# Optimization experiments

Measured on AMD Instinct MI355X. Metric: run time of the kernel, lower is better.

The kernel has to match this reference:

```python
import jax, jax.numpy as jnp
import numpy as np

B, S, D, H = 2, 2048, 1024, 16
DK = D // H
SCALE = 1.0 / np.sqrt(DK).astype(np.float32)


def setup_inputs() -> dict:
    key = jax.random.key(0)
    ks = jax.random.split(key, 7)
    std = 1.0 / np.sqrt(D).astype(np.float32)
    return {
        "query": jax.random.normal(ks[0], (B, S, D), jnp.float32),
        "key": jax.random.normal(ks[1], (B, S, D), jnp.float32),
        "value": jax.random.normal(ks[2], (B, S, D), jnp.float32),
        "Wq": jax.random.normal(ks[3], (D, D), jnp.float32) * std,
        "Wk": jax.random.normal(ks[4], (D, D), jnp.float32) * std,
        "Wv": jax.random.normal(ks[5], (D, D), jnp.float32) * std,
        "Wo": jax.random.normal(ks[6], (D, D), jnp.float32) * std,
    }


def _split_heads(x):
    # [B, S, D] -> [B, H, S, DK]
    return x.reshape(B, S, H, DK).transpose(0, 2, 1, 3)


def reference(query, key, value, Wq, Wk, Wv, Wo):
    Q = _split_heads(query @ Wq)
    K = _split_heads(key @ Wk)
    V = _split_heads(value @ Wv)
    # explicit full-score attention, as in the original (mask=None, dropout off)
    scores = jnp.einsum("bhqd,bhkd->bhqk", Q, K) * SCALE
    attn = jax.nn.softmax(scores, axis=-1)
    out = jnp.einsum("bhqk,bhkd->bhqd", attn, V)
    out = out.transpose(0, 2, 1, 3).reshape(B, S, D)  # merge heads
    return out @ Wo
```

## Files before the change

### kernel.cpp

```cpp
#include <hip/hip_runtime.h>

#define B_ 2
#define S_ 2048
#define D_ 1024
#define H_ 16

typedef unsigned short u16;
typedef unsigned long long u64;
typedef __bf16 bf16x8 __attribute__((ext_vector_type(8)));
typedef float f32x4 __attribute__((ext_vector_type(4)));
typedef unsigned short u16x8 __attribute__((ext_vector_type(8)));
typedef unsigned short u16x4 __attribute__((ext_vector_type(4)));
typedef unsigned uint4v __attribute__((ext_vector_type(4)));

__device__ __forceinline__ unsigned swz128(unsigned o) {
  return o ^ (((o >> 7) & 7) << 4);
}
__device__ __forceinline__ unsigned swz256(unsigned o) {
  return o ^ (((o >> 8) & 7) << 4);
}

__device__ __forceinline__ unsigned xcd_swz(unsigned id, unsigned cpx) {
  return (id & 7) * cpx + (id >> 3);
}

__device__ __forceinline__ void gload_lds16(const void* g, void* l) {
  __builtin_amdgcn_global_load_lds(
      (const __attribute__((address_space(1))) unsigned*)g,
      (__attribute__((address_space(3))) unsigned*)l, 16, 0, 0);
}

__device__ __forceinline__ u16 f2bf(float f) {
  union { float f; unsigned u; } v;
  v.f = f;
  unsigned u = v.u;
  return (u16)((u + 0x7fffu + ((u >> 16) & 1u)) >> 16);
}

__device__ __forceinline__ unsigned cvtpk(float lo, float hi) {
  unsigned d;
  asm("v_cvt_pk_bf16_f32 %0, %1, %2" : "=v"(d) : "v"(lo), "v"(hi));
  return d;
}

__device__ __forceinline__ float max3f(float a, float b, float c) {
  float d;
  asm("v_max3_f32 %0, %1, %2, %3" : "=v"(d) : "v"(a), "v"(b), "v"(c));
  return d;
}

struct T4 { const float* in[4]; u16* out[4]; };
__global__ __launch_bounds__(256) void transpose_w4(T4 p) {
  __shared__ u16 t[64][65];
  const float* in = p.in[blockIdx.z];
  u16* out = p.out[blockIdx.z];
  int r0 = blockIdx.y * 64, c0 = blockIdx.x * 64;
  for (int i = threadIdx.x; i < 4096; i += 256) {
    int r = i >> 6, c = i & 63;
    t[r][c] = f2bf(in[(size_t)(r0 + r) * 1024 + c0 + c]);
  }
  __syncthreads();
  for (int i = threadIdx.x; i < 4096; i += 256) {
    int r = i >> 6, c = i & 63;
    out[(size_t)(c0 + r) * 1024 + r0 + c] = t[c][r];
  }
}

struct QKV { const float* A[3]; const u16* BT[3]; u16* C[2]; u16* VT; };
__global__ __launch_bounds__(256) void gemm_qkv(QKV p) {
  constexpr int K = 1024, N = 1024;
  __shared__ __align__(16) u16 lbuf[2][128 * 64];
  const int tid = threadIdx.x, lane = tid & 63, w = tid >> 6;
  const int wr = w >> 1, wc = w & 1;
  const int z = blockIdx.z;
  const int m0 = blockIdx.x * 128, n0 = blockIdx.y * 128;
  const int g = lane >> 4, c16 = lane & 15;
  f32x4 acc[4][4] = {};
  const float* Af = p.A[z] + (size_t)m0 * K;
  const char* Bb = (const char*)(p.BT[z] + (size_t)n0 * K);
  char* lAb = (char*)lbuf[0];
  char* lBb = (char*)lbuf[1];
  for (int kt = 0; kt < K; kt += 64) {
    for (int c = 0; c < 4; ++c) {
      unsigned o = c * 4096 + tid * 16;
      unsigned u = swz128(o);
      gload_lds16(Bb + (size_t)(u >> 7) * (K * 2) + kt * 2 + (u & 127), lBb + o);
    }
    for (int c = 0; c < 4; ++c) {
      unsigned o = c * 4096 + tid * 16;
      unsigned row = o >> 7, kc = (o & 127) >> 1;
      const float* s = Af + (size_t)row * K + kt + kc;
      float4 f0 = *(const float4*)s;
      float4 f1 = *(const float4*)(s + 4);
      uint4v d;
      d[0] = cvtpk(f0.x, f0.y);
      d[1] = cvtpk(f0.z, f0.w);
      d[2] = cvtpk(f1.x, f1.y);
      d[3] = cvtpk(f1.z, f1.w);
      *(uint4v*)(lAb + swz128(o)) = d;
    }
    asm volatile("s_waitcnt vmcnt(0)" ::: "memory");
    __syncthreads();
    for (int ks = 0; ks < 2; ++ks) {
      bf16x8 af[4], bf[4];
      for (int i = 0; i < 4; ++i) {
        unsigned row = wr * 64 + i * 16 + c16;
        unsigned o = row * 128 + ks * 64 + g * 16;
        af[i] = *(const bf16x8*)(lAb + (o ^ ((row & 7) << 4)));
      }
      for (int j = 0; j < 4; ++j) {
        unsigned row = wc * 64 + j * 16 + c16;
        unsigned o = row * 128 + ks * 64 + g * 16;
        bf[j] = *(const bf16x8*)(lBb + (o ^ ((row & 7) << 4)));
      }
      for (int i = 0; i < 4; ++i)
        for (int j = 0; j < 4; ++j)
          acc[i][j] = __builtin_amdgcn_mfma_f32_16x16x32_bf16(af[i], bf[j],
                                                              acc[i][j], 0, 0, 0);
    }
    __syncthreads();
  }
  if (z < 2) {
    u16* C = p.C[z];
    for (int i = 0; i < 4; ++i)
      for (int j = 0; j < 4; ++j) {
        int row = m0 + wr * 64 + i * 16 + g * 4;
        int col = n0 + wc * 64 + j * 16 + c16;
        for (int r = 0; r < 4; ++r)
          C[(size_t)(row + r) * N + col] = f2bf(acc[i][j][r]);
      }
  } else {
    char* Tb = (char*)lbuf;
    for (int i = 0; i < 4; ++i)
      for (int j = 0; j < 4; ++j) {
        unsigned s_local = wr * 64 + i * 16 + g * 4;
        unsigned dk_col = wc * 64 + j * 16 + c16;
        unsigned o = dk_col * 256 + s_local * 2;
        u16x4 ov;
        ov[0] = f2bf(acc[i][j][0]);
        ov[1] = f2bf(acc[i][j][1]);
        ov[2] = f2bf(acc[i][j][2]);
        ov[3] = f2bf(acc[i][j][3]);
        *(u16x4*)(Tb + swz256(o)) = ov;
      }
    __syncthreads();
    const int b = m0 >> 11, s0blk = m0 & 2047;
    for (int c = 0; c < 8; ++c) {
      unsigned idx = c * 4096 + tid * 16;
      unsigned row = idx >> 8, off = idx & 255;
      int h = (n0 + (int)row) >> 6, dk = (n0 + (int)row) & 63;
      int bh = b * 16 + h;
      char* dst = (char*)p.VT + (((size_t)bh * 64 + dk) * S_ + s0blk) * 2 + off;
      *(u16x8*)dst = *(const u16x8*)(Tb + swz256(idx));
    }
  }
}

__global__ __launch_bounds__(256) void gemm_bt_f32(const u16* __restrict__ A,
                                                   const u16* __restrict__ BT,
                                                   float* __restrict__ C) {
  constexpr int K = 1024, N = 1024;
  __shared__ __align__(16) u16 lA[128 * 64];
  __shared__ __align__(16) u16 lB[64 * 64];
  const int tid = threadIdx.x, lane = tid & 63, w = tid >> 6;
  const int wr = w >> 1, wc = w & 1;
  const int m0 = blockIdx.x * 128, n0 = blockIdx.y * 64;
  const int g = lane >> 4, c16 = lane & 15;
  f32x4 acc[4][2] = {};
  const char* Ab = (const char*)(A + (size_t)m0 * K);
  const char* Bb = (const char*)(BT + (size_t)n0 * K);
  char* lAb = (char*)lA;
  char* lBb = (char*)lB;
  for (int kt = 0; kt < K; kt += 64) {
    for (int c = 0; c < 4; ++c) {
      unsigned o = w * 4096 + c * 1024 + lane * 16;
      unsigned u = swz128(o);
      gload_lds16(Ab + (size_t)(u >> 7) * (K * 2) + kt * 2 + (u & 127),
                  lAb + w * 4096 + c * 1024);
    }
    for (int c = 0; c < 2; ++c) {
      unsigned o = w * 2048 + c * 1024 + lane * 16;
      unsigned u = swz128(o);
      gload_lds16(Bb + (size_t)(u >> 7) * (K * 2) + kt * 2 + (u & 127),
                  lBb + w * 2048 + c * 1024);
    }
    asm volatile("s_waitcnt vmcnt(0)" ::: "memory");
    __syncthreads();
    for (int ks = 0; ks < 2; ++ks) {
      bf16x8 af[4], bf[2];
      for (int i = 0; i < 4; ++i) {
        unsigned row = wr * 64 + i * 16 + c16;
        unsigned o = row * 128 + ks * 64 + g * 16;
        af[i] = *(const bf16x8*)(lAb + (o ^ ((row & 7) << 4)));
      }
      for (int j = 0; j < 2; ++j) {
        unsigned row = wc * 32 + j * 16 + c16;
        unsigned o = row * 128 + ks * 64 + g * 16;
        bf[j] = *(const bf16x8*)(lBb + (o ^ ((row & 7) << 4)));
      }
      for (int i = 0; i < 4; ++i)
        for (int j = 0; j < 2; ++j)
          acc[i][j] = __builtin_amdgcn_mfma_f32_16x16x32_bf16(af[i], bf[j],
                                                              acc[i][j], 0, 0, 0);
    }
    __syncthreads();
  }
  for (int i = 0; i < 4; ++i)
    for (int j = 0; j < 2; ++j) {
      int row = m0 + wr * 64 + i * 16 + g * 4;
      int col = n0 + wc * 32 + j * 16 + c16;
      for (int r = 0; r < 4; ++r)
        C[(size_t)(row + r) * N + col] = acc[i][j][r];
    }
}

__global__ __launch_bounds__(256) void flash_attn(const u16* __restrict__ Q,
                                                  const u16* __restrict__ K,
                                                  const u16* __restrict__ VT,
                                                  u16* __restrict__ O) {
  __shared__ __align__(16) u16 lP[64 * 64];
  __shared__ __align__(16) u16 lK[2][64 * 64];
  __shared__ __align__(16) u16 lV[2][64 * 64];
  const int tid = threadIdx.x, lane = tid & 63, w = tid >> 6;
  const int g = lane >> 4, c16 = lane & 15;
  unsigned id = blockIdx.x + blockIdx.y * gridDim.x;
  unsigned sw = xcd_swz(id, 128);
  const int q0 = (sw & 31) * 64;
  const int bh = sw >> 5, b = bh >> 4, h = bh & 15;
  const char* Qb = (const char*)(Q + (size_t)(b * S_ + q0) * D_ + h * 64);
  const char* Kb = (const char*)(K + (size_t)b * S_ * D_ + h * 64);
  const char* Vb = (const char*)(VT + (size_t)bh * 64 * S_);
  char* lPb = (char*)lP;
  char* lKb = (char*)lK;
  char* lVb = (char*)lV;

  const unsigned mask = (c16 & 7) << 4;
  const unsigned fb0 = c16 * 128 + ((g * 16) ^ mask);
  const unsigned fb1 = c16 * 128 + ((64 + g * 16) ^ mask);
  unsigned uo[2];
  for (int c = 0; c < 2; ++c) uo[c] = swz128(w * 2048 + c * 1024 + lane * 16);

  for (int c = 0; c < 2; ++c) {
    unsigned u = uo[c];
    unsigned dst = w * 2048 + c * 1024;
    gload_lds16(Qb + (size_t)(u >> 7) * (D_ * 2) + (u & 127), lPb + dst);
    gload_lds16(Kb + (size_t)(u >> 7) * (D_ * 2) + (u & 127), lKb + dst);
    gload_lds16(Vb + (size_t)(u >> 7) * (S_ * 2) + (u & 127), lVb + dst);
  }
  float m_run = -INFINITY, l_run = 0.f;
  f32x4 oacc[4] = {};
  asm volatile("s_waitcnt vmcnt(0)" ::: "memory");
  __syncthreads();
  bf16x8 qf[2];
  qf[0] = *(const bf16x8*)(lPb + w * 2048 + fb0);
  qf[1] = *(const bf16x8*)(lPb + w * 2048 + fb1);
  const float SC2 = 0.125f * 1.44269504088896340736f;
  const unsigned qrow = w * 16 + c16;
  const unsigned pw = qrow * 128 + ((g * 8) ^ (mask & 16));
  const unsigned mh = mask & 96;
  int cur = 0;
  for (int kv0 = 0; kv0 < S_; kv0 += 64, cur ^= 1) {
    const char* curK = lKb + cur * 8192;
    const char* curV = lVb + cur * 8192;
    if (kv0 + 64 < S_) {
      char* nK = lKb + (cur ^ 1) * 8192;
      char* nV = lVb + (cur ^ 1) * 8192;
      for (int c = 0; c < 2; ++c) {
        unsigned u = uo[c];
        unsigned dst = w * 2048 + c * 1024;
        gload_lds16(Kb + (size_t)(kv0 + 64 + (u >> 7)) * (D_ * 2) + (u & 127),
                    nK + dst);
        gload_lds16(Vb + (size_t)(u >> 7) * (S_ * 2) + (size_t)(kv0 + 64) * 2 + (u & 127),
                    nV + dst);
      }
    }
    f32x4 s[4] = {};
    __builtin_amdgcn_s_setprio(1);
    for (int j = 0; j < 4; ++j) {
      bf16x8 kf = *(const bf16x8*)(curK + fb0 + j * 2048);
      s[j] = __builtin_amdgcn_mfma_f32_16x16x32_bf16(kf, qf[0], s[j], 0, 0, 0);
    }
    for (int j = 0; j < 4; ++j) {
      bf16x8 kf = *(const bf16x8*)(curK + fb1 + j * 2048);
      s[j] = __builtin_amdgcn_mfma_f32_16x16x32_bf16(kf, qf[1], s[j], 0, 0, 0);
    }
    __builtin_amdgcn_s_setprio(0);
    float t0 = max3f(s[0][0], s[0][1], s[0][2]);
    float t1 = max3f(s[0][3], s[1][0], s[1][1]);
    float t2 = max3f(s[1][2], s[1][3], s[2][0]);
    float t3 = max3f(s[2][1], s[2][2], s[2][3]);
    float t4 = max3f(s[3][0], s[3][1], s[3][2]);
    float rm = fmaxf(max3f(t0, t1, t2), max3f(t3, t4, s[3][3]));
    rm = fmaxf(rm, __shfl_xor(rm, 16));
    rm = fmaxf(rm, __shfl_xor(rm, 32));
    if (!__all((rm - m_run) * SC2 <= 8.0f)) {
      float mn = fmaxf(m_run, rm);
      float sc = exp2f((m_run - mn) * SC2);
      l_run *= sc;
      for (int i = 0; i < 4; ++i) oacc[i] *= sc;
      m_run = mn;
    }
    float rsj[4];
    for (int j = 0; j < 4; ++j) {
      float p0 = exp2f((s[j][0] - m_run) * SC2);
      float p1 = exp2f((s[j][1] - m_run) * SC2);
      float p2 = exp2f((s[j][2] - m_run) * SC2);
      float p3 = exp2f((s[j][3] - m_run) * SC2);
      rsj[j] = (p0 + p1) + (p2 + p3);
      unsigned w0 = cvtpk(p0, p1);
      unsigned w1 = cvtpk(p2, p3);
      *(u64*)(lPb + pw + ((unsigned)(j * 32) ^ mh)) = (u64)w0 | ((u64)w1 << 32);
    }
    l_run += (rsj[0] + rsj[1]) + (rsj[2] + rsj[3]);
    __builtin_amdgcn_s_setprio(1);
    {
      bf16x8 pf0 = *(const bf16x8*)(lPb + w * 2048 + fb0);
      for (int i = 0; i < 4; ++i) {
        bf16x8 vf = *(const bf16x8*)(curV + fb0 + i * 2048);
        oacc[i] = __builtin_amdgcn_mfma_f32_16x16x32_bf16(vf, pf0, oacc[i], 0, 0, 0);
      }
      bf16x8 pf1 = *(const bf16x8*)(lPb + w * 2048 + fb1);
      for (int i = 0; i < 4; ++i) {
        bf16x8 vf = *(const bf16x8*)(curV + fb1 + i * 2048);
        oacc[i] = __builtin_amdgcn_mfma_f32_16x16x32_bf16(vf, pf1, oacc[i], 0, 0, 0);
      }
    }
    __builtin_amdgcn_s_setprio(0);
    asm volatile("s_waitcnt vmcnt(0)" ::: "memory");
    __syncthreads();
  }
  l_run += __shfl_xor(l_run, 16);
  l_run += __shfl_xor(l_run, 32);
  float inv = 1.f / l_run;
  int q = q0 + w * 16 + c16;
  u16* orow = O + (size_t)(b * S_ + q) * D_ + h * 64;
  for (int i = 0; i < 4; ++i) {
    unsigned e0 = cvtpk(oacc[i][0] * inv, oacc[i][1] * inv);
    unsigned e1 = cvtpk(oacc[i][2] * inv, oacc[i][3] * inv);
    *(u64*)(orow + i * 16 + g * 4) = (u64)e0 | ((u64)e1 << 32);
  }
}

extern "C" void kernel_launch(void* const* d_in, const int* in_sizes, int n_in,
                              void* d_out, int out_size, void* d_ws, size_t ws_size,
                              hipStream_t stream) {
  const float* q_in = (const float*)d_in[0];
  const float* k_in = (const float*)d_in[1];
  const float* v_in = (const float*)d_in[2];
  const float* Wq = (const float*)d_in[3];
  const float* Wk = (const float*)d_in[4];
  const float* Wv = (const float*)d_in[5];
  const float* Wo = (const float*)d_in[6];
  u16* ws = (u16*)d_ws;
  const size_t WSZ = (size_t)1024 * 1024;
  const size_t TSZ = (size_t)B_ * S_ * D_;
  u16* WqT = ws;
  u16* WkT = ws + WSZ;
  u16* WvT = ws + 2 * WSZ;
  u16* WoT = ws + 3 * WSZ;
  u16* Qb = ws + 4 * WSZ;
  u16* Kb = Qb + TSZ;
  u16* VTb = Kb + TSZ;
  u16* Ob = VTb + TSZ;
  dim3 tb(256);
  T4 tw = {{Wq, Wk, Wv, Wo}, {WqT, WkT, WvT, WoT}};
  transpose_w4<<<dim3(16, 16, 4), tb, 0, stream>>>(tw);
  QKV gq = {{q_in, k_in, v_in}, {WqT, WkT, WvT}, {Qb, Kb}, VTb};
  gemm_qkv<<<dim3(32, 8, 3), tb, 0, stream>>>(gq);
  flash_attn<<<dim3(32, 32), tb, 0, stream>>>(Qb, Kb, VTb, Ob);
  gemm_bt_f32<<<dim3(32, 16), tb, 0, stream>>>(Ob, WoT, (float*)d_out);
}
```

Baseline: 153.7 us.

## Split attention KV range in two with a merge kernel, single-buffer LDS

Flash attention now splits each query tile's KV sequence into two halves processed by separate blocks, doubling the grid to 2048 blocks. Each block writes unnormalized partial outputs (bf16) and its running max and sum, and a new merge_o kernel combines the two halves and normalizes. K/V LDS staging drops from double-buffered prefetch to a single buffer loaded after compute with a full wait, which shrinks LDS per block. It targets better occupancy and CU fill, but adds a kernel launch, extra partial-output traffic, bf16 rounding of the unnormalized partials, and loses the load/compute overlap.

```diff
diff --git a/kernel.cpp b/kernel.cpp
--- a/kernel.cpp
+++ b/kernel.cpp
@@ -35,6 +35,12 @@
   v.f = f;
   unsigned u = v.u;
   return (u16)((u + 0x7fffu + ((u >> 16) & 1u)) >> 16);
+}
+
+__device__ __forceinline__ float bf2f(u16 x) {
+  union { unsigned u; float f; } v;
+  v.u = ((unsigned)x) << 16;
+  return v.f;
 }
 
 __device__ __forceinline__ unsigned cvtpk(float lo, float hi) {
@@ -217,16 +223,18 @@
 __global__ __launch_bounds__(256) void flash_attn(const u16* __restrict__ Q,
                                                   const u16* __restrict__ K,
                                                   const u16* __restrict__ VT,
-                                                  u16* __restrict__ O) {
+                                                  u16* __restrict__ pO,
+                                                  float2* __restrict__ pML) {
   __shared__ __align__(16) u16 lP[64 * 64];
-  __shared__ __align__(16) u16 lK[2][64 * 64];
-  __shared__ __align__(16) u16 lV[2][64 * 64];
+  __shared__ __align__(16) u16 lK[64 * 64];
+  __shared__ __align__(16) u16 lV[64 * 64];
   const int tid = threadIdx.x, lane = tid & 63, w = tid >> 6;
   const int g = lane >> 4, c16 = lane & 15;
-  unsigned id = blockIdx.x + blockIdx.y * gridDim.x;
-  unsigned sw = xcd_swz(id, 128);
+  unsigned sw = xcd_swz(blockIdx.x, 256);
   const int q0 = (sw & 31) * 64;
-  const int bh = sw >> 5, b = bh >> 4, h = bh & 15;
+  const int half = (sw >> 5) & 1;
+  const int bh = sw >> 6, b = bh >> 4, h = bh & 15;
+  const int kv_base = half * (S_ / 2);
   const char* Qb = (const char*)(Q + (size_t)(b * S_ + q0) * D_ + h * 64);
   const char* Kb = (const char*)(K + (size_t)b * S_ * D_ + h * 64);
   const char* Vb = (const char*)(VT + (size_t)bh * 64 * S_);
@@ -244,8 +252,8 @@
     unsigned u = uo[c];
     unsigned dst = w * 2048 + c * 1024;
     gload_lds16(Qb + (size_t)(u >> 7) * (D_ * 2) + (u & 127), lPb + dst);
-    gload_lds16(Kb + (size_t)(u >> 7) * (D_ * 2) + (u & 127), lKb + dst);
-    gload_lds16(Vb + (size_t)(u >> 7) * (S_ * 2) + (u & 127), lVb + dst);
+    gload_lds16(Kb + (size_t)(kv_base + (u >> 7)) * (D_ * 2) + (u & 127), lKb + dst);
+    gload_lds16(Vb + (size_t)(u >> 7) * (S_ * 2) + (size_t)kv_base * 2 + (u & 127), lVb + dst);
   }
   float m_run = -INFINITY, l_run = 0.f;
   f32x4 oacc[4] = {};
@@ -258,30 +266,15 @@
   const unsigned qrow = w * 16 + c16;
   const unsigned pw = qrow * 128 + ((g * 8) ^ (mask & 16));
   const unsigned mh = mask & 96;
-  int cur = 0;
-  for (int kv0 = 0; kv0 < S_; kv0 += 64, cur ^= 1) {
-    const char* curK = lKb + cur * 8192;
-    const char* curV = lVb + cur * 8192;
-    if (kv0 + 64 < S_) {
-      char* nK = lKb + (cur ^ 1) * 8192;
-      char* nV = lVb + (cur ^ 1) * 8192;
-      for (int c = 0; c < 2; ++c) {
-        unsigned u = uo[c];
-        unsigned dst = w * 2048 + c * 1024;
-        gload_lds16(Kb + (size_t)(kv0 + 64 + (u >> 7)) * (D_ * 2) + (u & 127),
-                    nK + dst);
-        gload_lds16(Vb + (size_t)(u >> 7) * (S_ * 2) + (size_t)(kv0 + 64) * 2 + (u & 127),
-                    nV + dst);
-      }
-    }
+  for (int t = 0; t < 16; ++t) {
     f32x4 s[4] = {};
     __builtin_amdgcn_s_setprio(1);
     for (int j = 0; j < 4; ++j) {
-      bf16x8 kf = *(const bf16x8*)(curK + fb0 + j * 2048);
+      bf16x8 kf = *(const bf16x8*)(lKb + fb0 + j * 2048);
       s[j] = __builtin_amdgcn_mfma_f32_16x16x32_bf16(kf, qf[0], s[j], 0, 0, 0);
     }
     for (int j = 0; j < 4; ++j) {
-      bf16x8 kf = *(const bf16x8*)(curK + fb1 + j * 2048);
+      bf16x8 kf = *(const bf16x8*)(lKb + fb1 + j * 2048);
       s[j] = __builtin_amdgcn_mfma_f32_16x16x32_bf16(kf, qf[1], s[j], 0, 0, 0);
     }
     __builtin_amdgcn_s_setprio(0);
@@ -300,45 +293,84 @@
       for (int i = 0; i < 4; ++i) oacc[i] *= sc;
       m_run = mn;
     }
-    float rsj[4];
     for (int j = 0; j < 4; ++j) {
       float p0 = exp2f((s[j][0] - m_run) * SC2);
       float p1 = exp2f((s[j][1] - m_run) * SC2);
       float p2 = exp2f((s[j][2] - m_run) * SC2);
       float p3 = exp2f((s[j][3] - m_run) * SC2);
-      rsj[j] = (p0 + p1) + (p2 + p3);
+      l_run += (p0 + p1) + (p2 + p3);
       unsigned w0 = cvtpk(p0, p1);
       unsigned w1 = cvtpk(p2, p3);
       *(u64*)(lPb + pw + ((unsigned)(j * 32) ^ mh)) = (u64)w0 | ((u64)w1 << 32);
     }
-    l_run += (rsj[0] + rsj[1]) + (rsj[2] + rsj[3]);
     __builtin_amdgcn_s_setprio(1);
     {
       bf16x8 pf0 = *(const bf16x8*)(lPb + w * 2048 + fb0);
       for (int i = 0; i < 4; ++i) {
-        bf16x8 vf = *(const bf16x8*)(curV + fb0 + i * 2048);
+        bf16x8 vf = *(const bf16x8*)(lVb + fb0 + i * 2048);
         oacc[i] = __builtin_amdgcn_mfma_f32_16x16x32_bf16(vf, pf0, oacc[i], 0, 0, 0);
       }
       bf16x8 pf1 = *(const bf16x8*)(lPb + w * 2048 + fb1);
       for (int i = 0; i < 4; ++i) {
-        bf16x8 vf = *(const bf16x8*)(curV + fb1 + i * 2048);
+        bf16x8 vf = *(const bf16x8*)(lVb + fb1 + i * 2048);
         oacc[i] = __builtin_amdgcn_mfma_f32_16x16x32_bf16(vf, pf1, oacc[i], 0, 0, 0);
       }
     }
     __builtin_amdgcn_s_setprio(0);
-    asm volatile("s_waitcnt vmcnt(0)" ::: "memory");
+    __syncthreads();
+    if (t < 15) {
+      int kv_next = kv_base + (t + 1) * 64;
+      for (int c = 0; c < 2; ++c) {
+        unsigned u = uo[c];
+        unsigned dst = w * 2048 + c * 1024;
+        gload_lds16(Kb + (size_t)(kv_next + (u >> 7)) * (D_ * 2) + (u & 127),
+                    lKb + dst);
+        gload_lds16(Vb + (size_t)(u >> 7) * (S_ * 2) + (size_t)kv_next * 2 + (u & 127),
+                    lVb + dst);
+      }
+      asm volatile("s_waitcnt vmcnt(0)" ::: "memory");
+    }
     __syncthreads();
   }
   l_run += __shfl_xor(l_run, 16);
   l_run += __shfl_xor(l_run, 32);
-  float inv = 1.f / l_run;
-  int q = q0 + w * 16 + c16;
-  u16* orow = O + (size_t)(b * S_ + q) * D_ + h * 64;
+  const size_t qr = (size_t)(half * 32 + bh) * S_ + (q0 + qrow);
+  u16* po = pO + qr * 64;
   for (int i = 0; i < 4; ++i) {
-    unsigned e0 = cvtpk(oacc[i][0] * inv, oacc[i][1] * inv);
-    unsigned e1 = cvtpk(oacc[i][2] * inv, oacc[i][3] * inv);
-    *(u64*)(orow + i * 16 + g * 4) = (u64)e0 | ((u64)e1 << 32);
-  }
+    unsigned e0 = cvtpk(oacc[i][0], oacc[i][1]);
+    unsigned e1 = cvtpk(oacc[i][2], oacc[i][3]);
+    *(u64*)(po + i * 16 + g * 4) = (u64)e0 | ((u64)e1 << 32);
+  }
+  if (g == 0) pML[qr] = make_float2(m_run, l_run);
+}
+
+__global__ __launch_bounds__(256) void merge_o(const u16* __restrict__ pO,
+                                               const float2* __restrict__ pML,
+                                               u16* __restrict__ Ob) {
+  const float SC2 = 0.125f * 1.44269504088896340736f;
+  int idx = blockIdx.x * 256 + threadIdx.x;
+  int qr = idx >> 3, sub = idx & 7;
+  float2 ml0 = pML[qr];
+  float2 ml1 = pML[65536 + qr];
+  float m = fmaxf(ml0.x, ml1.x);
+  float e0 = exp2f((ml0.x - m) * SC2);
+  float e1 = exp2f((ml1.x - m) * SC2);
+  float inv = 1.f / (ml0.y * e0 + ml1.y * e1);
+  e0 *= inv;
+  e1 *= inv;
+  u16x8 a = *((const u16x8*)pO + ((size_t)qr * 8 + sub));
+  u16x8 c = *((const u16x8*)pO + ((size_t)65536 * 8 + (size_t)qr * 8 + sub));
+  u16x8 o;
+  for (int e = 0; e < 8; e += 2) {
+    float lo = bf2f(a[e]) * e0 + bf2f(c[e]) * e1;
+    float hi = bf2f(a[e + 1]) * e0 + bf2f(c[e + 1]) * e1;
+    unsigned d = cvtpk(lo, hi);
+    o[e] = (u16)d;
+    o[e + 1] = (u16)(d >> 16);
+  }
+  int bh = qr >> 11, q = qr & 2047;
+  int b = bh >> 4, h = bh & 15;
+  *(u16x8*)(Ob + ((size_t)(b * S_ + q) * D_ + h * 64 + sub * 8)) = o;
 }
 
 extern "C" void kernel_launch(void* const* d_in, const int* in_sizes, int n_in,
@@ -361,12 +393,15 @@
   u16* Qb = ws + 4 * WSZ;
   u16* Kb = Qb + TSZ;
   u16* VTb = Kb + TSZ;
-  u16* Ob = VTb + TSZ;
+  u16* pO = VTb + TSZ;
+  float2* pML = (float2*)(pO + 2 * TSZ);
+  u16* Ob = pO + 2 * TSZ + 524288;
   dim3 tb(256);
   T4 tw = {{Wq, Wk, Wv, Wo}, {WqT, WkT, WvT, WoT}};
   transpose_w4<<<dim3(16, 16, 4), tb, 0, stream>>>(tw);
   QKV gq = {{q_in, k_in, v_in}, {WqT, WkT, WvT}, {Qb, Kb}, VTb};
   gemm_qkv<<<dim3(32, 8, 3), tb, 0, stream>>>(gq);
-  flash_attn<<<dim3(32, 32), tb, 0, stream>>>(Qb, Kb, VTb, Ob);
+  flash_attn<<<dim3(2048), tb, 0, stream>>>(Qb, Kb, VTb, pO, pML);
+  merge_o<<<dim3(2048), tb, 0, stream>>>(pO, pML, Ob);
   gemm_bt_f32<<<dim3(32, 16), tb, 0, stream>>>(Ob, WoT, (float*)d_out);
 }
```

After: 156.2 us. Within noise of the previous version (+1.6%).
